# Optimization experiments

Hardware: AMD Instinct MI355X
Metric: run time of the kernel (lower is better)

## Reference

```python
import jax, jax.numpy as jnp
import numpy as np

J, N, C = 24, 131072, 16
GS = (128, 128, 128)
MAT = ((0, 1), (0, 2), (1, 2))  # matMode
VEC = (2, 1, 0)                 # vecMode


def _bilinear(plane, xy):
    # plane: (C, H, W); xy: (N, 2) in [-1, 1]; align_corners=True grid_sample
    Cc, H, W = plane.shape
    x = (xy[:, 0] + 1.0) * 0.5 * (W - 1)
    y = (xy[:, 1] + 1.0) * 0.5 * (H - 1)
    x0 = jnp.clip(jnp.floor(x), 0, W - 1)
    y0 = jnp.clip(jnp.floor(y), 0, H - 1)
    x1 = jnp.clip(x0 + 1, 0, W - 1)
    y1 = jnp.clip(y0 + 1, 0, H - 1)
    wx = x - x0
    wy = y - y0
    x0i, x1i, y0i, y1i = (a.astype(jnp.int32) for a in (x0, x1, y0, y1))
    v00 = plane[:, y0i, x0i]  # (C, N)
    v01 = plane[:, y0i, x1i]
    v10 = plane[:, y1i, x0i]
    v11 = plane[:, y1i, x1i]
    top = v00 * (1.0 - wx) + v01 * wx
    bot = v10 * (1.0 - wx) + v11 * wx
    return top * (1.0 - wy) + bot * wy  # (C, N)


def _linear1d(line, z):
    # line: (C, L); z: (N,) in [-1, 1]; 1D version (grid x coord is 0, width 1)
    Cc, L = line.shape
    y = (z + 1.0) * 0.5 * (L - 1)
    y0 = jnp.clip(jnp.floor(y), 0, L - 1)
    y1 = jnp.clip(y0 + 1, 0, L - 1)
    wy = y - y0
    v0 = line[:, y0.astype(jnp.int32)]  # (C, N)
    v1 = line[:, y1.astype(jnp.int32)]
    return v0 * (1.0 - wy) + v1 * wy


def setup_inputs() -> dict:
    key = jax.random.key(0)
    ks = jax.random.split(key, 7)
    xyz = jax.random.uniform(ks[0], (J, N, 3), jnp.float32) * 2.0 - 1.0
    scale = 1.0
    def p_init(k, shape):
        return -(scale * 0.5) + 0.1 + scale * jax.random.normal(k, shape, jnp.float32)
    inp = {"xyz_sampled": xyz}
    for i in range(3):
        m0, m1 = MAT[i]
        inp[f"plane{i}"] = p_init(ks[1 + i], (J, C, GS[m1], GS[m0]))
        inp[f"line{i}"] = p_init(ks[4 + i], (J, C, GS[VEC[i]]))
    return inp


def reference(xyz_sampled, plane0, plane1, plane2, line0, line1, line2):
    planes = (plane0, plane1, plane2)
    lines = (line0, line1, line2)
    feat = jnp.zeros(xyz_sampled.shape[:2], xyz_sampled.dtype)  # (J, N)
    for i in range(3):
        xy = jnp.stack([xyz_sampled[..., MAT[i][0]], xyz_sampled[..., MAT[i][1]]], axis=-1)  # (J,N,2)
        p = jax.vmap(_bilinear)(planes[i], xy)                 # (J, C, N)
        l = jax.vmap(_linear1d)(lines[i], xyz_sampled[..., VEC[i]])  # (J, C, N)
        feat = feat + jnp.sum(p * l, axis=1)
    return jax.nn.relu(feat)
```

## Files before the change

### kernel.cpp

```cpp
#include <hip/hip_runtime.h>
#include <hip/hip_fp16.h>
#include <stdint.h>

#define JB 24
#define NP 131072
#define CH 16
#define G  128
#define NPTS (JB*NP)

#define PLANE_H2 (JB*G*G*CH)
#define LINE_H2  (JB*G*CH)

typedef _Float16 h2_t __attribute__((ext_vector_type(2)));
typedef unsigned int u32x4 __attribute__((ext_vector_type(4)));

__device__ __forceinline__ float fdot2(uint32_t a, h2_t w, float c) {
#if __has_builtin(__builtin_amdgcn_fdot2)
    return __builtin_amdgcn_fdot2(__builtin_bit_cast(h2_t, a), w, c, false);
#else
    __half2 ha = __builtin_bit_cast(__half2, a);
    float2 fa = __half22float2(ha);
    h2_t wv = w;
    return c + fa.x * (float)wv[0] + fa.y * (float)wv[1];
#endif
}

__global__ __launch_bounds__(256)
void pack_planes_kernel(const float* __restrict__ p0,
                        const float* __restrict__ p1,
                        const float* __restrict__ p2,
                        __half2* __restrict__ wsp) {
    __shared__ float lds[CH * (G + 1)];
    int b = blockIdx.x;
    int y = b & (G - 1);
    int j = (b >> 7) % JB;
    int p = b / (G * JB);
    const float* src = (p == 0 ? p0 : (p == 1 ? p1 : p2))
                       + ((size_t)j * CH) * (G * G) + (size_t)y * G;
    __half2* dst = wsp + ((size_t)(p * JB + j) * G + y) * (G * CH);
    int tid = threadIdx.x;
    for (int idx = tid; idx < G * CH; idx += 256) {
        int c = idx >> 7;
        int x = idx & (G - 1);
        lds[c * (G + 1) + x] = src[(size_t)c * G * G + x];
    }
    __syncthreads();
    for (int idx = tid; idx < G * CH; idx += 256) {
        int x = idx >> 4;
        int c = idx & 15;
        int x1 = (x < G - 1) ? x + 1 : x;
        float a = lds[c * (G + 1) + x];
        float bvv = lds[c * (G + 1) + x1];
        dst[idx] = __floats2half2_rn(a, bvv);
    }
}

__global__ __launch_bounds__(256)
void pack_lines_kernel(const float* __restrict__ l0,
                       const float* __restrict__ l1,
                       const float* __restrict__ l2,
                       __half2* __restrict__ wsl) {
    int gid = blockIdx.x * 256 + threadIdx.x;
    if (gid >= 3 * LINE_H2) return;
    int p = gid / LINE_H2;
    int r = gid - p * LINE_H2;
    int j = r >> 11;
    int z = (r >> 4) & (G - 1);
    int c = r & 15;
    int z1 = (z < G - 1) ? z + 1 : z;
    const float* src = (p == 0 ? l0 : (p == 1 ? l1 : l2));
    float a = src[((size_t)j * CH + c) * G + z];
    float bvv = src[((size_t)j * CH + c) * G + z1];
    wsl[gid] = __floats2half2_rn(a, bvv);
}

__global__ __launch_bounds__(1024)
void tensorf_lds1k_kernel(const float* __restrict__ xyz,
                          const uint32_t* __restrict__ wp,
                          const uint32_t* __restrict__ wl,
                          float* __restrict__ out) {
    const int NWG = NPTS / 1024;
    int bid = blockIdx.x;
    int wg = (bid & 7) * (NWG >> 3) + (bid >> 3);
    int tid = threadIdx.x;
    int ptblk = wg << 10;
    int j = ptblk >> 17;

    __shared__ uint32_t slines[3 * 2048];
    {
        u32x4* dst4 = (u32x4*)slines;
        for (int idx = tid; idx < 1536; idx += 1024) {
            int i = idx >> 9;
            int r = idx & 511;
            dst4[idx] = ((const u32x4*)(wl + (((size_t)i * JB + j) << 11)))[r];
        }
    }
    __syncthreads();

    int l4 = tid & 3;
    int slot = tid >> 2;

    #pragma unroll
    for (int p = 0; p < 4; ++p) {
        int pt = ptblk + (p << 8) + slot;

        float cx = xyz[(size_t)pt * 3 + 0];
        float cy = xyz[(size_t)pt * 3 + 1];
        float cz = xyz[(size_t)pt * 3 + 2];

        float fa = (cx + 1.f) * 63.5f;
        float fb = (cy + 1.f) * 63.5f;
        float fc = (cz + 1.f) * 63.5f;
        float f0a = floorf(fa), f0b = floorf(fb), f0c = floorf(fc);
        int ia = (int)f0a, ib = (int)f0b, ic = (int)f0c;
        float wa = fa - f0a, wb = fb - f0b, wc = fc - f0c;
        h2_t wah = {(_Float16)(1.f - wa), (_Float16)wa};
        h2_t wbh = {(_Float16)(1.f - wb), (_Float16)wb};
        h2_t wch = {(_Float16)(1.f - wc), (_Float16)wc};

        const int   X0[3] = {ia, ia, ib};
        const int   Y0[3] = {ib, ic, ic};
        const int   Z0[3] = {ic, ib, ia};
        const h2_t  WX[3] = {wah, wah, wbh};
        const float WY[3] = {wb, wc, wc};
        const h2_t  WZ[3] = {wch, wbh, wah};

        float4 acc = {0.f, 0.f, 0.f, 0.f};
        #pragma unroll
        for (int i = 0; i < 3; ++i) {
            int pb = ((i * JB + j) << 18) + (((Y0[i] << 7) + X0[i]) << 4) + (l4 << 2);
            u32x4 A = *(const u32x4*)(wp + pb);
            u32x4 B = *(const u32x4*)(wp + pb + (G << 4));
            u32x4 C = *(const u32x4*)(slines + (i << 11) + (Z0[i] << 4) + (l4 << 2));
            h2_t wxh = WX[i], wzh = WZ[i];
            float wy = WY[i];

            float t0 = fdot2(A.x, wxh, 0.f);
            float t1 = fdot2(A.y, wxh, 0.f);
            float t2 = fdot2(A.z, wxh, 0.f);
            float t3 = fdot2(A.w, wxh, 0.f);
            float b0 = fdot2(B.x, wxh, 0.f);
            float b1 = fdot2(B.y, wxh, 0.f);
            float b2 = fdot2(B.z, wxh, 0.f);
            float b3 = fdot2(B.w, wxh, 0.f);
            float v0 = fdot2(C.x, wzh, 0.f);
            float v1 = fdot2(C.y, wzh, 0.f);
            float v2 = fdot2(C.z, wzh, 0.f);
            float v3 = fdot2(C.w, wzh, 0.f);
            float q0 = t0 + (b0 - t0) * wy;
            float q1 = t1 + (b1 - t1) * wy;
            float q2 = t2 + (b2 - t2) * wy;
            float q3 = t3 + (b3 - t3) * wy;
            acc.x = fmaf(q0, v0, acc.x);
            acc.y = fmaf(q1, v1, acc.y);
            acc.z = fmaf(q2, v2, acc.z);
            acc.w = fmaf(q3, v3, acc.w);
        }
        float s = (acc.x + acc.y) + (acc.z + acc.w);
        s += __shfl_xor(s, 1);
        s += __shfl_xor(s, 2);
        if (l4 == 0) out[pt] = fmaxf(s, 0.f);
    }
}

__global__ __launch_bounds__(256)
void tensorf_direct_kernel(const float* __restrict__ xyz,
                           const float* __restrict__ p0,
                           const float* __restrict__ p1,
                           const float* __restrict__ p2,
                           const float* __restrict__ l0,
                           const float* __restrict__ l1,
                           const float* __restrict__ l2,
                           float* __restrict__ out) {
    int gid = blockIdx.x * 256 + threadIdx.x;
    if (gid >= NPTS) return;
    int j = gid >> 17;
    float cx = xyz[(size_t)gid * 3 + 0];
    float cy = xyz[(size_t)gid * 3 + 1];
    float cz = xyz[(size_t)gid * 3 + 2];
    const float co[3] = {cx, cy, cz};
    const int M0[3] = {0, 0, 1};
    const int M1[3] = {1, 2, 2};
    const int VZ[3] = {2, 1, 0};
    const float* PP[3] = {p0, p1, p2};
    const float* LL[3] = {l0, l1, l2};

    float acc = 0.f;
    #pragma unroll
    for (int i = 0; i < 3; ++i) {
        float fx = (co[M0[i]] + 1.f) * 63.5f;
        float fy = (co[M1[i]] + 1.f) * 63.5f;
        float fz = (co[VZ[i]] + 1.f) * 63.5f;
        float f0x = fminf(fmaxf(floorf(fx), 0.f), 127.f);
        float f0y = fminf(fmaxf(floorf(fy), 0.f), 127.f);
        float f0z = fminf(fmaxf(floorf(fz), 0.f), 127.f);
        int x0 = (int)f0x, y0 = (int)f0y, z0 = (int)f0z;
        int x1 = min(x0 + 1, G - 1);
        int y1 = min(y0 + 1, G - 1);
        int z1 = min(z0 + 1, G - 1);
        float wx = fx - f0x, wy = fy - f0y, wz = fz - f0z;

        const float* p = PP[i] + (size_t)j * CH * G * G;
        const float* l = LL[i] + (size_t)j * CH * G;
        for (int c = 0; c < CH; ++c) {
            const float* pc = p + (size_t)c * G * G;
            float v00 = pc[(size_t)y0 * G + x0];
            float v01 = pc[(size_t)y0 * G + x1];
            float v10 = pc[(size_t)y1 * G + x0];
            float v11 = pc[(size_t)y1 * G + x1];
            float lc0 = l[(size_t)c * G + z0];
            float lc1 = l[(size_t)c * G + z1];
            float top = v00 + (v01 - v00) * wx;
            float bot = v10 + (v11 - v10) * wx;
            float pv  = top + (bot - top) * wy;
            float lv  = lc0 + (lc1 - lc0) * wz;
            acc += pv * lv;
        }
    }
    out[gid] = fmaxf(acc, 0.f);
}

extern "C" void kernel_launch(void* const* d_in, const int* in_sizes, int n_in,
                              void* d_out, int out_size, void* d_ws, size_t ws_size,
                              hipStream_t stream) {
    const float* xyz = (const float*)d_in[0];
    const float* p0  = (const float*)d_in[1];
    const float* l0  = (const float*)d_in[2];
    const float* p1  = (const float*)d_in[3];
    const float* l1  = (const float*)d_in[4];
    const float* p2  = (const float*)d_in[5];
    const float* l2  = (const float*)d_in[6];
    float* out = (float*)d_out;

    const size_t need = ((size_t)3 * PLANE_H2 + (size_t)3 * LINE_H2) * sizeof(__half2);

    if (ws_size >= need) {
        __half2* wsp = (__half2*)d_ws;
        __half2* wsl = wsp + (size_t)3 * PLANE_H2;
        pack_planes_kernel<<<3 * JB * G, 256, 0, stream>>>(p0, p1, p2, wsp);
        pack_lines_kernel<<<(3 * LINE_H2 + 255) / 256, 256, 0, stream>>>(l0, l1, l2, wsl);
        tensorf_lds1k_kernel<<<NPTS / 1024, 1024, 0, stream>>>(
            xyz, (const uint32_t*)wsp, (const uint32_t*)wsl, out);
    } else {
        tensorf_direct_kernel<<<(NPTS + 255) / 256, 256, 0, stream>>>(xyz, p0, p1, p2, l0, l1, l2, out);
    }
}
```

Before: 120.7 us.

## Software-pipeline plane gathers with inline-asm loads and explicit vmcnt waits

Replaces the per-point gather loop with a two-stage software pipeline. All xyz coordinates are loaded up front, then the six plane dwordx4 gathers for the next point are issued through inline asm while the current point is computed, using s_waitcnt vmcnt(6) to wait only on the older batch. The aim is to keep more global loads in flight per wave and hide gather latency. In exchange it holds twelve 128-bit registers live, which raises VGPR pressure at 1024 threads per block. It also depends on vmcnt ordering being right, and the xyz loads issued earlier must already have retired.

```diff
diff --git a/kernel.cpp b/kernel.cpp
--- a/kernel.cpp
+++ b/kernel.cpp
@@ -74,11 +74,90 @@
     wsl[gid] = __floats2half2_rn(a, bvv);
 }
 
+template<int Q>
+__device__ __forceinline__ void issue_pt(u32x4 (&R)[2][6],
+                                         float fa, float fb, float fc,
+                                         int j, int l4, const uint32_t* wp) {
+    float f0a = floorf(fa), f0b = floorf(fb), f0c = floorf(fc);
+    int ia = (int)f0a, ib = (int)f0b, ic = (int)f0c;
+    const int X0[3] = {ia, ia, ib};
+    const int Y0[3] = {ib, ic, ic};
+    #pragma unroll
+    for (int i = 0; i < 3; ++i) {
+        int pb = ((i * JB + j) << 18) + (((Y0[i] << 7) + X0[i]) << 4) + (l4 << 2);
+        uint64_t a0 = (uint64_t)(wp + pb);
+        uint64_t a1 = a0 + 8192;
+        asm volatile("global_load_dwordx4 %0, %1, off" : "=v"(R[Q][2*i])     : "v"(a0));
+        asm volatile("global_load_dwordx4 %0, %1, off" : "=v"(R[Q][2*i + 1]) : "v"(a1));
+    }
+}
+
+template<int Q>
+__device__ __forceinline__ void wait_vm6(u32x4 (&R)[2][6]) {
+    asm volatile("s_waitcnt vmcnt(6)"
+        : "+v"(R[Q][0]), "+v"(R[Q][1]), "+v"(R[Q][2]),
+          "+v"(R[Q][3]), "+v"(R[Q][4]), "+v"(R[Q][5]));
+}
+template<int Q>
+__device__ __forceinline__ void wait_vm0(u32x4 (&R)[2][6]) {
+    asm volatile("s_waitcnt vmcnt(0)"
+        : "+v"(R[Q][0]), "+v"(R[Q][1]), "+v"(R[Q][2]),
+          "+v"(R[Q][3]), "+v"(R[Q][4]), "+v"(R[Q][5]));
+}
+
+template<int Q>
+__device__ __forceinline__ float compute_pt(u32x4 (&R)[2][6],
+                                            float fa, float fb, float fc,
+                                            const uint32_t* slines, int l4) {
+    float f0a = floorf(fa), f0b = floorf(fb), f0c = floorf(fc);
+    float wa = fa - f0a, wb = fb - f0b, wc = fc - f0c;
+    int ia = (int)f0a, ib = (int)f0b, ic = (int)f0c;
+    h2_t wah = {(_Float16)(1.f - wa), (_Float16)wa};
+    h2_t wbh = {(_Float16)(1.f - wb), (_Float16)wb};
+    h2_t wch = {(_Float16)(1.f - wc), (_Float16)wc};
+    const int   Z0[3] = {ic, ib, ia};
+    const h2_t  WX[3] = {wah, wah, wbh};
+    const float WY[3] = {wb, wc, wc};
+    const h2_t  WZ[3] = {wch, wbh, wah};
+
+    float4 acc = {0.f, 0.f, 0.f, 0.f};
+    #pragma unroll
+    for (int i = 0; i < 3; ++i) {
+        u32x4 A = R[Q][2*i];
+        u32x4 B = R[Q][2*i + 1];
+        u32x4 C = *(const u32x4*)(slines + (i << 11) + (Z0[i] << 4) + (l4 << 2));
+        h2_t wxh = WX[i], wzh = WZ[i];
+        float wy = WY[i];
+
+        float t0 = fdot2(A.x, wxh, 0.f);
+        float t1 = fdot2(A.y, wxh, 0.f);
+        float t2 = fdot2(A.z, wxh, 0.f);
+        float t3 = fdot2(A.w, wxh, 0.f);
+        float b0 = fdot2(B.x, wxh, 0.f);
+        float b1 = fdot2(B.y, wxh, 0.f);
+        float b2 = fdot2(B.z, wxh, 0.f);
+        float b3 = fdot2(B.w, wxh, 0.f);
+        float v0 = fdot2(C.x, wzh, 0.f);
+        float v1 = fdot2(C.y, wzh, 0.f);
+        float v2 = fdot2(C.z, wzh, 0.f);
+        float v3 = fdot2(C.w, wzh, 0.f);
+        float q0 = t0 + (b0 - t0) * wy;
+        float q1 = t1 + (b1 - t1) * wy;
+        float q2 = t2 + (b2 - t2) * wy;
+        float q3 = t3 + (b3 - t3) * wy;
+        acc.x = fmaf(q0, v0, acc.x);
+        acc.y = fmaf(q1, v1, acc.y);
+        acc.z = fmaf(q2, v2, acc.z);
+        acc.w = fmaf(q3, v3, acc.w);
+    }
+    return (acc.x + acc.y) + (acc.z + acc.w);
+}
+
 __global__ __launch_bounds__(1024)
-void tensorf_lds1k_kernel(const float* __restrict__ xyz,
-                          const uint32_t* __restrict__ wp,
-                          const uint32_t* __restrict__ wl,
-                          float* __restrict__ out) {
+void tensorf_pipe_kernel(const float* __restrict__ xyz,
+                         const uint32_t* __restrict__ wp,
+                         const uint32_t* __restrict__ wl,
+                         float* __restrict__ out) {
     const int NWG = NPTS / 1024;
     int bid = blockIdx.x;
     int wg = (bid & 7) * (NWG >> 3) + (bid >> 3);
@@ -100,66 +179,34 @@
     int l4 = tid & 3;
     int slot = tid >> 2;
 
+    float fa[4], fb[4], fc[4];
     #pragma unroll
     for (int p = 0; p < 4; ++p) {
         int pt = ptblk + (p << 8) + slot;
-
-        float cx = xyz[(size_t)pt * 3 + 0];
-        float cy = xyz[(size_t)pt * 3 + 1];
-        float cz = xyz[(size_t)pt * 3 + 2];
-
-        float fa = (cx + 1.f) * 63.5f;
-        float fb = (cy + 1.f) * 63.5f;
-        float fc = (cz + 1.f) * 63.5f;
-        float f0a = floorf(fa), f0b = floorf(fb), f0c = floorf(fc);
-        int ia = (int)f0a, ib = (int)f0b, ic = (int)f0c;
-        float wa = fa - f0a, wb = fb - f0b, wc = fc - f0c;
-        h2_t wah = {(_Float16)(1.f - wa), (_Float16)wa};
-        h2_t wbh = {(_Float16)(1.f - wb), (_Float16)wb};
-        h2_t wch = {(_Float16)(1.f - wc), (_Float16)wc};
-
-        const int   X0[3] = {ia, ia, ib};
-        const int   Y0[3] = {ib, ic, ic};
-        const int   Z0[3] = {ic, ib, ia};
-        const h2_t  WX[3] = {wah, wah, wbh};
-        const float WY[3] = {wb, wc, wc};
-        const h2_t  WZ[3] = {wch, wbh, wah};
-
-        float4 acc = {0.f, 0.f, 0.f, 0.f};
-        #pragma unroll
-        for (int i = 0; i < 3; ++i) {
-            int pb = ((i * JB + j) << 18) + (((Y0[i] << 7) + X0[i]) << 4) + (l4 << 2);
-            u32x4 A = *(const u32x4*)(wp + pb);
-            u32x4 B = *(const u32x4*)(wp + pb + (G << 4));
-            u32x4 C = *(const u32x4*)(slines + (i << 11) + (Z0[i] << 4) + (l4 << 2));
-            h2_t wxh = WX[i], wzh = WZ[i];
-            float wy = WY[i];
-
-            float t0 = fdot2(A.x, wxh, 0.f);
-            float t1 = fdot2(A.y, wxh, 0.f);
-            float t2 = fdot2(A.z, wxh, 0.f);
-            float t3 = fdot2(A.w, wxh, 0.f);
-            float b0 = fdot2(B.x, wxh, 0.f);
-            float b1 = fdot2(B.y, wxh, 0.f);
-            float b2 = fdot2(B.z, wxh, 0.f);
-            float b3 = fdot2(B.w, wxh, 0.f);
-            float v0 = fdot2(C.x, wzh, 0.f);
-            float v1 = fdot2(C.y, wzh, 0.f);
-            float v2 = fdot2(C.z, wzh, 0.f);
-            float v3 = fdot2(C.w, wzh, 0.f);
-            float q0 = t0 + (b0 - t0) * wy;
-            float q1 = t1 + (b1 - t1) * wy;
-            float q2 = t2 + (b2 - t2) * wy;
-            float q3 = t3 + (b3 - t3) * wy;
-            acc.x = fmaf(q0, v0, acc.x);
-            acc.y = fmaf(q1, v1, acc.y);
-            acc.z = fmaf(q2, v2, acc.z);
-            acc.w = fmaf(q3, v3, acc.w);
-        }
-        float s = (acc.x + acc.y) + (acc.z + acc.w);
-        s += __shfl_xor(s, 1);
-        s += __shfl_xor(s, 2);
-        if (l4 == 0) out[pt] = fmaxf(s, 0.f);
+        fa[p] = (xyz[(size_t)pt * 3 + 0] + 1.f) * 63.5f;
+        fb[p] = (xyz[(size_t)pt * 3 + 1] + 1.f) * 63.5f;
+        fc[p] = (xyz[(size_t)pt * 3 + 2] + 1.f) * 63.5f;
+    }
+    __builtin_amdgcn_sched_barrier(0);
+
+    u32x4 R[2][6];
+    float s[4];
+
+    issue_pt<0>(R, fa[0], fb[0], fc[0], j, l4, wp);
+    issue_pt<1>(R, fa[1], fb[1], fc[1], j, l4, wp);
+    wait_vm6<0>(R); s[0] = compute_pt<0>(R, fa[0], fb[0], fc[0], slines, l4);
+    issue_pt<0>(R, fa[2], fb[2], fc[2], j, l4, wp);
+    wait_vm6<1>(R); s[1] = compute_pt<1>(R, fa[1], fb[1], fc[1], slines, l4);
+    issue_pt<1>(R, fa[3], fb[3], fc[3], j, l4, wp);
+    wait_vm6<0>(R); s[2] = compute_pt<0>(R, fa[2], fb[2], fc[2], slines, l4);
+    wait_vm0<1>(R); s[3] = compute_pt<1>(R, fa[3], fb[3], fc[3], slines, l4);
+
+    #pragma unroll
+    for (int p = 0; p < 4; ++p) {
+        float v = s[p];
+        v += __shfl_xor(v, 1);
+        v += __shfl_xor(v, 2);
+        if (l4 == 0) out[ptblk + (p << 8) + slot] = fmaxf(v, 0.f);
     }
 }
 
@@ -239,7 +286,7 @@
         __half2* wsl = wsp + (size_t)3 * PLANE_H2;
         pack_planes_kernel<<<3 * JB * G, 256, 0, stream>>>(p0, p1, p2, wsp);
         pack_lines_kernel<<<(3 * LINE_H2 + 255) / 256, 256, 0, stream>>>(l0, l1, l2, wsl);
-        tensorf_lds1k_kernel<<<NPTS / 1024, 1024, 0, stream>>>(
+        tensorf_pipe_kernel<<<NPTS / 1024, 1024, 0, stream>>>(
             xyz, (const uint32_t*)wsp, (const uint32_t*)wsl, out);
     } else {
         tensorf_direct_kernel<<<(NPTS + 255) / 256, 256, 0, stream>>>(xyz, p0, p1, p2, l0, l1, l2, out);
```

Result: slower. 143.6 us (+19.0%).
